# Optimization experiments

Hardware: AMD Instinct MI355X
Metric: run time of the kernel (lower is better)

## Reference

```python
import jax, jax.numpy as jnp
import numpy as np

B, T, L, W = 4, 4096, 64, 8          # batch, text len, media tokens, max_window_per_audio
DIM, DIM_A, H, DH = 2048, 1024, 8, 64
INNER = H * DH
LN_EPS = 1e-5


def setup_inputs() -> dict:
    key = jax.random.key(0)
    ks = jax.random.split(key, 8)
    x = jax.random.normal(ks[0], (B, T, DIM), jnp.float32)
    media = jax.random.normal(ks[1], (B, L, 1, DIM_A), jnp.float32)
    media_mask = jax.random.uniform(ks[2], (B, L, 1)) > 0.1
    # sparse media markers (~8 per row); ensure at least one per row
    media_locations = (jax.random.uniform(ks[3], (B, T)) < (8.0 / T)).astype(jnp.int32)
    media_locations = media_locations.at[:, 0].set(1)
    Wq = jax.random.normal(ks[4], (DIM, INNER), jnp.float32) / np.sqrt(DIM).astype(np.float32)
    Wkv = jax.random.normal(ks[5], (DIM_A, 2 * INNER), jnp.float32) / np.sqrt(DIM_A).astype(np.float32)
    Wout = jax.random.normal(ks[6], (INNER, DIM), jnp.float32) / np.sqrt(INNER).astype(np.float32)
    gamma = jnp.ones((DIM,), jnp.float32)
    beta = jnp.zeros((DIM,), jnp.float32)
    return dict(x=x, media=media, media_mask=media_mask, media_locations=media_locations,
                Wq=Wq, Wkv=Wkv, Wout=Wout, gamma=gamma, beta=beta)


def reference(x, media, media_mask, media_locations, Wq, Wkv, Wout, gamma, beta):
    scale = DH ** -0.5
    # LayerNorm (biased variance, like torch)
    mu = x.mean(-1, keepdims=True)
    var = x.var(-1, keepdims=True)
    xn = (x - mu) * jax.lax.rsqrt(var + LN_EPS) * gamma + beta
    # projections
    q = (xn @ Wq).reshape(B, T, H, DH).transpose(0, 2, 1, 3) * scale   # [B,h,T,dh]
    kv = media.reshape(B, L, DIM_A) @ Wkv
    k, v = jnp.split(kv, 2, axis=-1)
    k = k.reshape(B, L, H, DH).transpose(0, 2, 1, 3)                   # [B,h,L,dh]
    v = v.reshape(B, L, H, DH).transpose(0, 2, 1, 3)
    sim = jnp.einsum('bhid,bhjd->bhij', q, k)                          # [B,h,T,L]
    big = jnp.finfo(sim.dtype).max
    # media validity mask
    mm = media_mask.reshape(B, 1, 1, L)
    sim = jnp.where(mm, sim, -big)
    # few-shot window mask (only_attend_immediate_media=False):
    # token t attends windows [0, max(#media at <=t, 1) * W)
    cum = jnp.cumsum((media_locations != 0).astype(jnp.int32), axis=1)  # [B,T]
    end = jnp.maximum(cum, 1) * W                                       # [B,T]
    fsm = jnp.arange(L)[None, None, :] < end[:, :, None]                # [B,T,L]
    sim = jnp.where(fsm[:, None], sim, -big)
    sim = sim - jax.lax.stop_gradient(sim.max(-1, keepdims=True))
    attn = jax.nn.softmax(sim, axis=-1)
    out = jnp.einsum('bhij,bhjd->bhid', attn, v)                        # [B,h,T,dh]
    out = out.transpose(0, 2, 1, 3).reshape(B, T, INNER)
    return out @ Wout
```

## Files before the change

### kernel.cpp

```cpp
#include <hip/hip_runtime.h>
#include <float.h>

typedef __bf16 bf16;
typedef __bf16 bf16x8 __attribute__((ext_vector_type(8)));
typedef float f32x4 __attribute__((ext_vector_type(4)));

#define GAS __attribute__((address_space(1)))
#define LAS __attribute__((address_space(3)))

__device__ __forceinline__ void gload_lds16(const void* g, void* l) {
  __builtin_amdgcn_global_load_lds((const GAS unsigned int*)g, (LAS unsigned int*)l, 16, 0, 0);
}

template <int OUT_BF16>
__global__ __launch_bounds__(256, 2) void gemm_bt(
    const bf16* __restrict__ A, const bf16* __restrict__ Bt,
    void* __restrict__ Cv, int M, int N, int K) {
  __shared__ bf16 As[128 * 32];
  __shared__ bf16 Bs[128 * 32];
  const int tid = threadIdx.x;
  const int lane = tid & 63, w = tid >> 6;
  const int wr = w >> 1, wc = w & 1;

  const int gx = gridDim.x;
  const int nwg = gx * gridDim.y;
  int lid = blockIdx.y * gx + blockIdx.x;
  {
    const int qq = nwg >> 3, rr = nwg & 7;
    const int xcd = lid & 7, pos = lid >> 3;
    lid = (xcd < rr ? xcd * (qq + 1) : rr * (qq + 1) + (xcd - rr) * qq) + pos;
  }
  const int bx = lid % gx, by = lid / gx;
  const size_t m0 = (size_t)by * 128, n0 = (size_t)bx * 128;

  const int srow = lane >> 2, sslot = lane & 3;
  const int g = lane >> 4, fr = lane & 15;

  f32x4 acc[4][4] = {};

  for (int kt = 0; kt < K; kt += 32) {
    __syncthreads();
#pragma unroll
    for (int j = 0; j < 2; ++j) {
      const int c = 2 * w + j;
      const int r = c * 16 + srow;
      const int ks = (sslot ^ (r & 3)) << 3;
      gload_lds16(A + (m0 + r) * K + kt + ks, &As[c * 512]);
      gload_lds16(Bt + (n0 + r) * K + kt + ks, &Bs[c * 512]);
    }
    __syncthreads();
    bf16x8 av[4], bv[4];
#pragma unroll
    for (int mi = 0; mi < 4; ++mi) {
      const int r = wr * 64 + mi * 16 + fr;
      av[mi] = *(const bf16x8*)&As[r * 32 + ((g ^ (r & 3)) << 3)];
    }
#pragma unroll
    for (int ni = 0; ni < 4; ++ni) {
      const int r = wc * 64 + ni * 16 + fr;
      bv[ni] = *(const bf16x8*)&Bs[r * 32 + ((g ^ (r & 3)) << 3)];
    }
#pragma unroll
    for (int mi = 0; mi < 4; ++mi)
#pragma unroll
      for (int ni = 0; ni < 4; ++ni)
        acc[mi][ni] = __builtin_amdgcn_mfma_f32_16x16x32_bf16(
            av[mi], bv[ni], acc[mi][ni], 0, 0, 0);
  }

#pragma unroll
  for (int mi = 0; mi < 4; ++mi)
#pragma unroll
    for (int ni = 0; ni < 4; ++ni)
#pragma unroll
      for (int rg = 0; rg < 4; ++rg) {
        const size_t row = m0 + wr * 64 + mi * 16 + g * 4 + rg;
        const size_t col = n0 + wc * 64 + ni * 16 + fr;
        if (OUT_BF16)
          ((bf16*)Cv)[row * (size_t)N + col] = (bf16)acc[mi][ni][rg];
        else
          ((float*)Cv)[row * (size_t)N + col] = acc[mi][ni][rg];
      }
}

__global__ __launch_bounds__(256) void prep_all(
    const float* __restrict__ x, const float* __restrict__ gamma,
    const float* __restrict__ beta, bf16* __restrict__ xn,
    const float* __restrict__ Wq, bf16* __restrict__ wqT,
    const float* __restrict__ Wkv, bf16* __restrict__ wkvT,
    const float* __restrict__ Wout, bf16* __restrict__ woT,
    const float* __restrict__ media, bf16* __restrict__ medb,
    const int* __restrict__ mloc, int* __restrict__ endw,
    const unsigned char* __restrict__ mraw, int* __restrict__ mk) {
  __shared__ float shf[256];
  const int blk = blockIdx.x, tid = threadIdx.x;

  if (blk < 16384) {
    const size_t base = (size_t)blk * 2048 + tid * 8;
    f32x4 v0 = *(const f32x4*)(x + base);
    f32x4 v1 = *(const f32x4*)(x + base + 4);
    float s = 0.f, q2 = 0.f;
#pragma unroll
    for (int j = 0; j < 4; ++j) {
      s += v0[j] + v1[j];
      q2 += v0[j] * v0[j] + v1[j] * v1[j];
    }
    for (int off = 32; off > 0; off >>= 1) {
      s += __shfl_down(s, off);
      q2 += __shfl_down(q2, off);
    }
    const int lane = tid & 63, wv = tid >> 6;
    if (lane == 0) { shf[wv] = s; shf[4 + wv] = q2; }
    __syncthreads();
    s = shf[0] + shf[1] + shf[2] + shf[3];
    q2 = shf[4] + shf[5] + shf[6] + shf[7];
    const float mu = s * (1.f / 2048.f);
    const float var = q2 * (1.f / 2048.f) - mu * mu;
    const float rs = rsqrtf(var + 1e-5f);
    f32x4 g0 = *(const f32x4*)(gamma + tid * 8);
    f32x4 g1 = *(const f32x4*)(gamma + tid * 8 + 4);
    f32x4 b0 = *(const f32x4*)(beta + tid * 8);
    f32x4 b1 = *(const f32x4*)(beta + tid * 8 + 4);
    bf16x8 o;
#pragma unroll
    for (int j = 0; j < 4; ++j) {
      o[j] = (bf16)((v0[j] - mu) * rs * g0[j] + b0[j]);
      o[4 + j] = (bf16)((v1[j] - mu) * rs * g1[j] + b1[j]);
    }
    *(bf16x8*)(xn + base) = o;
  } else if (blk < 20480) {
    const int idx = (blk - 16384) * 256 + tid;
    const int c = idx >> 11, r = idx & 2047;
    wqT[idx] = (bf16)(Wq[(size_t)r * 512 + c] * 0.125f);
  } else if (blk < 24576) {
    const int idx = (blk - 20480) * 256 + tid;
    const int c = idx >> 10, r = idx & 1023;
    wkvT[idx] = (bf16)Wkv[(size_t)r * 1024 + c];
  } else if (blk < 28672) {
    const int idx = (blk - 24576) * 256 + tid;
    const int c = idx >> 9, r = idx & 511;
    woT[idx] = (bf16)Wout[(size_t)r * 2048 + c];
  } else if (blk < 29696) {
    const int i = (blk - 28672) * 256 + tid;
    medb[i] = (bf16)media[i];
  } else if (blk < 29700) {
    int* part = (int*)shf;
    const int b = blk - 29696;
    int loc[16];
    int s = 0;
    const int base = b * 4096 + tid * 16;
#pragma unroll
    for (int j = 0; j < 16; ++j) {
      loc[j] = (mloc[base + j] != 0) ? 1 : 0;
      s += loc[j];
    }
    part[tid] = s;
    __syncthreads();
    for (int off = 1; off < 256; off <<= 1) {
      int v = (tid >= off) ? part[tid - off] : 0;
      __syncthreads();
      part[tid] += v;
      __syncthreads();
    }
    int c = (tid > 0) ? part[tid - 1] : 0;
#pragma unroll
    for (int j = 0; j < 16; ++j) {
      c += loc[j];
      int e = (c > 1 ? c : 1) << 3;
      endw[base + j] = e > 64 ? 64 : e;
    }
  } else {
    int* isbool = (int*)shf;
    if (tid == 0) *isbool = 0;
    __syncthreads();
    const unsigned char v = mraw[tid];
    if ((tid & 3) != 0 && v != 0) atomicOr(isbool, 1);
    __syncthreads();
    mk[tid] = (*isbool) ? (int)mraw[tid] : ((const int*)mraw)[tid];
  }
}

__global__ __launch_bounds__(256, 2) void attn_kernel(
    const bf16* __restrict__ q, const bf16* __restrict__ kv,
    const int* __restrict__ mk, const int* __restrict__ endw,
    bf16* __restrict__ ao) {
  __shared__ bf16 Ks[64 * 64], Vs[64 * 64], Ps[64 * 64];
  __shared__ int mks[64];
  const int tid = threadIdx.x, lane = tid & 63, w = tid >> 6;
  const int b = blockIdx.z, h = blockIdx.y, t0 = blockIdx.x * 64;

#pragma unroll
  for (int s0 = 0; s0 < 2; ++s0) {
    const int sidx = s0 * 256 + tid;
    const int r = sidx >> 3, sl = sidx & 7;
    *(bf16x8*)&Ks[r * 64 + ((sl ^ (r & 7)) << 3)] =
        *(const bf16x8*)&kv[(size_t)(b * 64 + r) * 1024 + h * 64 + sl * 8];
    bf16x8 vv =
        *(const bf16x8*)&kv[(size_t)(b * 64 + r) * 1024 + 512 + h * 64 + sl * 8];
#pragma unroll
    for (int j = 0; j < 8; ++j) {
      const int dh = sl * 8 + j;
      Vs[dh * 64 + ((((r >> 3) ^ (dh & 7)) << 3) | (r & 7))] = vv[j];
    }
  }
  if (tid < 64) mks[tid] = mk[b * 64 + tid];
  __syncthreads();

  const int g = lane >> 4, fr = lane & 15;
  bf16x8 aq[2];
#pragma unroll
  for (int kg = 0; kg < 2; ++kg)
    aq[kg] = *(const bf16x8*)&q[(size_t)(b * 4096 + t0 + w * 16 + fr) * 512 +
                                h * 64 + kg * 32 + g * 8];
  f32x4 sacc[4] = {};
#pragma unroll
  for (int kg = 0; kg < 2; ++kg)
#pragma unroll
    for (int ni = 0; ni < 4; ++ni) {
      const int r = ni * 16 + fr;
      bf16x8 bk = *(const bf16x8*)&Ks[r * 64 + (((kg * 4 + g) ^ (r & 7)) << 3)];
      sacc[ni] = __builtin_amdgcn_mfma_f32_16x16x32_bf16(aq[kg], bk, sacc[ni],
                                                         0, 0, 0);
    }

  const int4 ev4 = *(const int4*)&endw[b * 4096 + t0 + w * 16 + g * 4];
  const int ev[4] = {ev4.x, ev4.y, ev4.z, ev4.w};
  float p[4][4];
#pragma unroll
  for (int ni = 0; ni < 4; ++ni) {
    const int l = ni * 16 + fr;
    const bool mv = (mks[l] != 0);
#pragma unroll
    for (int rg = 0; rg < 4; ++rg)
      p[ni][rg] = (mv && (l < ev[rg])) ? sacc[ni][rg] : -FLT_MAX;
  }
#pragma unroll
  for (int rg = 0; rg < 4; ++rg) {
    float m = fmaxf(fmaxf(p[0][rg], p[1][rg]), fmaxf(p[2][rg], p[3][rg]));
    m = fmaxf(m, __shfl_xor(m, 1));
    m = fmaxf(m, __shfl_xor(m, 2));
    m = fmaxf(m, __shfl_xor(m, 4));
    m = fmaxf(m, __shfl_xor(m, 8));
    float sum = 0.f;
#pragma unroll
    for (int ni = 0; ni < 4; ++ni) {
      p[ni][rg] = __expf(p[ni][rg] - m);
      sum += p[ni][rg];
    }
    sum += __shfl_xor(sum, 1);
    sum += __shfl_xor(sum, 2);
    sum += __shfl_xor(sum, 4);
    sum += __shfl_xor(sum, 8);
    const float inv = 1.f / sum;
#pragma unroll
    for (int ni = 0; ni < 4; ++ni) p[ni][rg] *= inv;
  }
#pragma unroll
  for (int ni = 0; ni < 4; ++ni) {
    const int l = ni * 16 + fr;
#pragma unroll
    for (int rg = 0; rg < 4; ++rg) {
      const int tr = w * 16 + g * 4 + rg;
      Ps[tr * 64 + ((((l >> 3) ^ (tr & 7)) << 3) | (l & 7))] = (bf16)p[ni][rg];
    }
  }
  __syncthreads();

  bf16x8 pa[2];
#pragma unroll
  for (int kg = 0; kg < 2; ++kg) {
    const int r = w * 16 + fr;
    pa[kg] = *(const bf16x8*)&Ps[r * 64 + (((kg * 4 + g) ^ (r & 7)) << 3)];
  }
  f32x4 oacc[4] = {};
#pragma unroll
  for (int kg = 0; kg < 2; ++kg)
#pragma unroll
    for (int ni = 0; ni < 4; ++ni) {
      const int r = ni * 16 + fr;
      bf16x8 bv = *(const bf16x8*)&Vs[r * 64 + (((kg * 4 + g) ^ (r & 7)) << 3)];
      oacc[ni] = __builtin_amdgcn_mfma_f32_16x16x32_bf16(pa[kg], bv, oacc[ni],
                                                         0, 0, 0);
    }
#pragma unroll
  for (int ni = 0; ni < 4; ++ni)
#pragma unroll
    for (int rg = 0; rg < 4; ++rg)
      ao[(size_t)(b * 4096 + t0 + w * 16 + g * 4 + rg) * 512 + h * 64 +
         ni * 16 + fr] = (bf16)oacc[ni][rg];
}

extern "C" void kernel_launch(void* const* d_in, const int* in_sizes, int n_in,
                              void* d_out, int out_size, void* d_ws,
                              size_t ws_size, hipStream_t stream) {
  const float* x = (const float*)d_in[0];
  const float* media = (const float*)d_in[1];
  const unsigned char* mraw = (const unsigned char*)d_in[2];
  const int* mloc = (const int*)d_in[3];
  const float* Wq = (const float*)d_in[4];
  const float* Wkv = (const float*)d_in[5];
  const float* Wout = (const float*)d_in[6];
  const float* gamma = (const float*)d_in[7];
  const float* beta = (const float*)d_in[8];
  float* out = (float*)d_out;

  bf16* xn = (bf16*)d_out;

  char* ws = (char*)d_ws;
  size_t off = 0;
  auto carve = [&](size_t bytes) {
    void* p = ws + off;
    off += (bytes + 255) & ~(size_t)255;
    return p;
  };
  bf16* qb = (bf16*)carve((size_t)16384 * 512 * 2);
  bf16* aob = (bf16*)carve((size_t)16384 * 512 * 2);
  bf16* kvb = (bf16*)carve((size_t)256 * 1024 * 2);
  bf16* wqT = (bf16*)carve((size_t)512 * 2048 * 2);
  bf16* wkvT = (bf16*)carve((size_t)1024 * 1024 * 2);
  bf16* woT = (bf16*)carve((size_t)2048 * 512 * 2);
  bf16* medb = (bf16*)carve((size_t)256 * 1024 * 2);
  int* endw = (int*)carve((size_t)4 * 4096 * 4);
  int* mk = (int*)carve(256 * 4);
  (void)ws_size;
  (void)in_sizes;
  (void)n_in;
  (void)out_size;

  prep_all<<<29701, 256, 0, stream>>>(x, gamma, beta, xn, Wq, wqT, Wkv, wkvT,
                                      Wout, woT, media, medb, mloc, endw, mraw,
                                      mk);

  gemm_bt<1><<<dim3(8, 2), 256, 0, stream>>>(medb, wkvT, kvb, 256, 1024, 1024);

  gemm_bt<1><<<dim3(4, 128), 256, 0, stream>>>(xn, wqT, qb, 16384, 512, 2048);

  attn_kernel<<<dim3(64, 8, 4), 256, 0, stream>>>(qb, kvb, mk, endw, aob);

  gemm_bt<0><<<dim3(16, 128), 256, 0, stream>>>(aob, woT, out, 16384, 2048, 512);
}
```

Baseline: 186.1 us.

## Add 4-stage pipelined 256-row GEMM and tiled weight transposes

Adds a new gemm_pipe kernel with 512 threads, 256xBN tiles, a 4-deep LDS ring buffer fed by direct global-to-LDS loads, XOR-swizzled LDS layout, explicit vmcnt waits and priority hints. It replaces the Q projection and output projection GEMMs. Separately, the weight transposes in the prep kernel now use 64x64 LDS-tiled transposes instead of strided per-element gathers, which cuts the block count. The larger tiles give more reuse and better overlap of loads with MFMA, but they raise LDS and register pressure and reduce grid size, which could hurt occupancy.

```diff
diff --git a/kernel.cpp b/kernel.cpp
--- a/kernel.cpp
+++ b/kernel.cpp
@@ -10,6 +10,151 @@
 
 __device__ __forceinline__ void gload_lds16(const void* g, void* l) {
   __builtin_amdgcn_global_load_lds((const GAS unsigned int*)g, (LAS unsigned int*)l, 16, 0, 0);
+}
+
+template <int OUT_BF16, int BN>
+__global__ __launch_bounds__(512, 2) void gemm_pipe(
+    const bf16* __restrict__ A, const bf16* __restrict__ Bt,
+    void* __restrict__ Cv, int M, int N, int K) {
+  constexpr int NR = BN / 64;
+  __shared__ __align__(16) bf16 Abuf[4][256 * 32];
+  __shared__ __align__(16) bf16 Bbuf[4][BN * 32];
+  const int tid = threadIdx.x, lane = tid & 63, w = tid >> 6;
+  const int wr = w >> 2, wc = w & 3;
+  const int g = lane >> 4, fr = lane & 15;
+
+  const int gx = gridDim.x;
+  const int nwg = gx * gridDim.y;
+  int lid = blockIdx.y * gx + blockIdx.x;
+  {
+    const int qq = nwg >> 3, rr = nwg & 7;
+    const int xcd = lid & 7, pos = lid >> 3;
+    lid = (xcd < rr ? xcd * (qq + 1) : rr * (qq + 1) + (xcd - rr) * qq) + pos;
+  }
+  const int bx = lid % gx, by = lid / gx;
+  const size_t m0 = (size_t)by * 256, n0 = (size_t)bx * BN;
+
+  const int nt = K >> 5;
+  const int srow = w * 16 + (lane >> 2);
+  const int sdslot = lane & 3;
+
+  auto stageA = [&](int t) {
+    const int q = t & 3;
+    const int kt = t << 5;
+#pragma unroll
+    for (int c = 0; c < 2; ++c) {
+      const int r = c * 128 + srow;
+      const int ss = sdslot ^ ((r >> 1) & 3);
+      gload_lds16(A + (m0 + r) * (size_t)K + kt + ss * 8,
+                  &Abuf[q][c * 4096 + w * 512]);
+    }
+  };
+  auto stageB = [&](int t) {
+    const int q = t & 3;
+    const int kt = t << 5;
+#pragma unroll
+    for (int c = 0; c < BN / 128; ++c) {
+      const int r = c * 128 + srow;
+      const int ss = sdslot ^ ((r >> 1) & 3);
+      gload_lds16(Bt + (n0 + r) * (size_t)K + kt + ss * 8,
+                  &Bbuf[q][c * 4096 + w * 512]);
+    }
+  };
+  auto rdA = [&](int q, int mi) {
+    const int r = wr * 128 + mi * 16 + fr;
+    return *(const bf16x8*)&Abuf[q][r * 32 + ((g ^ ((r >> 1) & 3)) << 3)];
+  };
+  auto rdB = [&](int q, int ni) {
+    const int r = wc * (BN / 4) + ni * 16 + fr;
+    return *(const bf16x8*)&Bbuf[q][r * 32 + ((g ^ ((r >> 1) & 3)) << 3)];
+  };
+
+  f32x4 acc[8][NR] = {};
+
+#pragma unroll
+  for (int t = 0; t < 4; ++t) {
+    stageA(t);
+    stageB(t);
+  }
+
+  const int body = nt - 4;
+  for (int t = 0; t < body; ++t) {
+    const int q = t & 3;
+    if constexpr (BN == 256)
+      asm volatile("s_waitcnt vmcnt(12)" ::: "memory");
+    else
+      asm volatile("s_waitcnt vmcnt(9)" ::: "memory");
+    __builtin_amdgcn_s_barrier();
+    __builtin_amdgcn_sched_barrier(0);
+
+    bf16x8 bv[NR], av0[4];
+#pragma unroll
+    for (int ni = 0; ni < NR; ++ni) bv[ni] = rdB(q, ni);
+#pragma unroll
+    for (int mi = 0; mi < 4; ++mi) av0[mi] = rdA(q, mi);
+    __builtin_amdgcn_s_setprio(1);
+#pragma unroll
+    for (int mi = 0; mi < 4; ++mi)
+#pragma unroll
+      for (int ni = 0; ni < NR; ++ni)
+        acc[mi][ni] = __builtin_amdgcn_mfma_f32_16x16x32_bf16(
+            av0[mi], bv[ni], acc[mi][ni], 0, 0, 0);
+    __builtin_amdgcn_s_setprio(0);
+    __builtin_amdgcn_s_barrier();
+    __builtin_amdgcn_sched_barrier(0);
+    stageB(t + 4);
+
+    bf16x8 av1[4];
+#pragma unroll
+    for (int mi = 0; mi < 4; ++mi) av1[mi] = rdA(q, 4 + mi);
+    __builtin_amdgcn_s_setprio(1);
+#pragma unroll
+    for (int mi = 0; mi < 4; ++mi)
+#pragma unroll
+      for (int ni = 0; ni < NR; ++ni)
+        acc[4 + mi][ni] = __builtin_amdgcn_mfma_f32_16x16x32_bf16(
+            av1[mi], bv[ni], acc[4 + mi][ni], 0, 0, 0);
+    __builtin_amdgcn_s_setprio(0);
+    __builtin_amdgcn_s_barrier();
+    __builtin_amdgcn_sched_barrier(0);
+    stageA(t + 4);
+  }
+
+  asm volatile("s_waitcnt vmcnt(0)" ::: "memory");
+  __builtin_amdgcn_s_barrier();
+  __builtin_amdgcn_sched_barrier(0);
+  for (int t = body; t < nt; ++t) {
+    const int q = t & 3;
+    bf16x8 bv[NR];
+#pragma unroll
+    for (int ni = 0; ni < NR; ++ni) bv[ni] = rdB(q, ni);
+#pragma unroll
+    for (int mh = 0; mh < 2; ++mh) {
+      bf16x8 av[4];
+#pragma unroll
+      for (int mi = 0; mi < 4; ++mi) av[mi] = rdA(q, mh * 4 + mi);
+#pragma unroll
+      for (int mi = 0; mi < 4; ++mi)
+#pragma unroll
+        for (int ni = 0; ni < NR; ++ni)
+          acc[mh * 4 + mi][ni] = __builtin_amdgcn_mfma_f32_16x16x32_bf16(
+              av[mi], bv[ni], acc[mh * 4 + mi][ni], 0, 0, 0);
+    }
+  }
+
+#pragma unroll
+  for (int mi = 0; mi < 8; ++mi)
+#pragma unroll
+    for (int ni = 0; ni < NR; ++ni)
+#pragma unroll
+      for (int rg = 0; rg < 4; ++rg) {
+        const size_t row = m0 + wr * 128 + mi * 16 + g * 4 + rg;
+        const size_t col = n0 + wc * (BN / 4) + ni * 16 + fr;
+        if (OUT_BF16)
+          ((bf16*)Cv)[row * (size_t)N + col] = (bf16)acc[mi][ni][rg];
+        else
+          ((float*)Cv)[row * (size_t)N + col] = acc[mi][ni][rg];
+      }
 }
 
 template <int OUT_BF16>
@@ -83,6 +228,27 @@
       }
 }
 
+__device__ __forceinline__ void transp64(const float* __restrict__ src,
+                                         bf16* __restrict__ dst, int R, int C,
+                                         float scale, int tile, float* lds) {
+  const int tilesC = C >> 6;
+  const int tr = tile / tilesC, tc = tile % tilesC;
+  const int r0 = tr << 6, c0 = tc << 6;
+  const int tid = threadIdx.x;
+  const int lr = tid >> 6, lc = tid & 63;
+#pragma unroll
+  for (int j = 0; j < 16; ++j) {
+    const int r = j * 4 + lr;
+    lds[r * 65 + lc] = src[(size_t)(r0 + r) * C + c0 + lc];
+  }
+  __syncthreads();
+#pragma unroll
+  for (int j = 0; j < 16; ++j) {
+    const int rr = j * 4 + lr;
+    dst[(size_t)(c0 + rr) * R + r0 + lc] = (bf16)(lds[lc * 65 + rr] * scale);
+  }
+}
+
 __global__ __launch_bounds__(256) void prep_all(
     const float* __restrict__ x, const float* __restrict__ gamma,
     const float* __restrict__ beta, bf16* __restrict__ xn,
@@ -92,7 +258,7 @@
     const float* __restrict__ media, bf16* __restrict__ medb,
     const int* __restrict__ mloc, int* __restrict__ endw,
     const unsigned char* __restrict__ mraw, int* __restrict__ mk) {
-  __shared__ float shf[256];
+  __shared__ float shf[64 * 65];
   const int blk = blockIdx.x, tid = threadIdx.x;
 
   if (blk < 16384) {
@@ -128,24 +294,18 @@
       o[4 + j] = (bf16)((v1[j] - mu) * rs * g1[j] + b1[j]);
     }
     *(bf16x8*)(xn + base) = o;
-  } else if (blk < 20480) {
-    const int idx = (blk - 16384) * 256 + tid;
-    const int c = idx >> 11, r = idx & 2047;
-    wqT[idx] = (bf16)(Wq[(size_t)r * 512 + c] * 0.125f);
-  } else if (blk < 24576) {
-    const int idx = (blk - 20480) * 256 + tid;
-    const int c = idx >> 10, r = idx & 1023;
-    wkvT[idx] = (bf16)Wkv[(size_t)r * 1024 + c];
-  } else if (blk < 28672) {
-    const int idx = (blk - 24576) * 256 + tid;
-    const int c = idx >> 9, r = idx & 511;
-    woT[idx] = (bf16)Wout[(size_t)r * 2048 + c];
-  } else if (blk < 29696) {
-    const int i = (blk - 28672) * 256 + tid;
+  } else if (blk < 16640) {
+    transp64(Wq, wqT, 2048, 512, 0.125f, blk - 16384, shf);
+  } else if (blk < 16896) {
+    transp64(Wkv, wkvT, 1024, 1024, 1.f, blk - 16640, shf);
+  } else if (blk < 17152) {
+    transp64(Wout, woT, 512, 2048, 1.f, blk - 16896, shf);
+  } else if (blk < 18176) {
+    const int i = (blk - 17152) * 256 + tid;
     medb[i] = (bf16)media[i];
-  } else if (blk < 29700) {
+  } else if (blk < 18180) {
     int* part = (int*)shf;
-    const int b = blk - 29696;
+    const int b = blk - 18176;
     int loc[16];
     int s = 0;
     const int base = b * 4096 + tid * 16;
@@ -327,15 +487,17 @@
   (void)n_in;
   (void)out_size;
 
-  prep_all<<<29701, 256, 0, stream>>>(x, gamma, beta, xn, Wq, wqT, Wkv, wkvT,
+  prep_all<<<18181, 256, 0, stream>>>(x, gamma, beta, xn, Wq, wqT, Wkv, wkvT,
                                       Wout, woT, media, medb, mloc, endw, mraw,
                                       mk);
 
   gemm_bt<1><<<dim3(8, 2), 256, 0, stream>>>(medb, wkvT, kvb, 256, 1024, 1024);
 
-  gemm_bt<1><<<dim3(4, 128), 256, 0, stream>>>(xn, wqT, qb, 16384, 512, 2048);
+  gemm_pipe<1, 128><<<dim3(4, 64), 512, 0, stream>>>(xn, wqT, qb, 16384, 512,
+                                                     2048);
 
   attn_kernel<<<dim3(64, 8, 4), 256, 0, stream>>>(qb, kvb, mk, endw, aob);
 
-  gemm_bt<0><<<dim3(16, 128), 256, 0, stream>>>(aob, woT, out, 16384, 2048, 512);
-}
+  gemm_pipe<0, 256><<<dim3(8, 64), 512, 0, stream>>>(aob, woT, out, 16384,
+                                                     2048, 512);
+}
```

After: 193.3 us. +3.9%, slower.
